# Performance work log

Hardware: AMD Instinct MI355X
Metric: run time of the kernel (lower is better)

Reference implementation:

```python
import jax, jax.numpy as jnp
import numpy as np

N_NODES = 50000
N_EDGES = 1600000
NEG_SLOPE = 0.2


def setup_inputs() -> dict:
    key = jax.random.key(0)
    ks = jax.random.split(key, 11)
    s = 0.1  # small init scale
    return {
        "x": jax.random.normal(ks[0], (N_NODES, 128), dtype=jnp.float32),
        "edge_index": jax.random.randint(ks[1], (2, N_EDGES), 0, N_NODES, dtype=jnp.int64),
        "W1": jax.random.normal(ks[2], (128, 128), dtype=jnp.float32) * s,
        "att_src1": jax.random.normal(ks[3], (2, 64), dtype=jnp.float32) * s,
        "att_dst1": jax.random.normal(ks[4], (2, 64), dtype=jnp.float32) * s,
        "b1": jax.random.normal(ks[5], (128,), dtype=jnp.float32) * s,
        "W2": jax.random.normal(ks[6], (128, 64), dtype=jnp.float32) * s,
        "att_src2": jax.random.normal(ks[7], (1, 64), dtype=jnp.float32) * s,
        "att_dst2": jax.random.normal(ks[8], (1, 64), dtype=jnp.float32) * s,
        "b2": jax.random.normal(ks[9], (64,), dtype=jnp.float32) * s,
    }


def gat_conv(x, W, a_src, a_dst, bias, src, dst, n_nodes):
    # x: [N, F_in]; W: [F_in, H*C]; a_src/a_dst: [H, C]; bias: [H*C]
    H, C = a_src.shape
    xl = (x @ W).reshape(n_nodes, H, C)                 # [N,H,C]
    alpha_s = jnp.einsum('nhc,hc->nh', xl, a_src)       # [N,H]
    alpha_d = jnp.einsum('nhc,hc->nh', xl, a_dst)       # [N,H]
    e = jax.nn.leaky_relu(alpha_s[src] + alpha_d[dst], NEG_SLOPE)  # [E,H]
    # segment softmax over edges sharing the same destination node
    m = jax.ops.segment_max(e, dst, num_segments=n_nodes)          # [N,H]
    m = jnp.where(jnp.isfinite(m), m, 0.0)
    e = jnp.exp(e - m[dst])
    denom = jax.ops.segment_sum(e, dst, num_segments=n_nodes)      # [N,H]
    alpha = e / denom[dst]                               # self-loops guarantee denom > 0
    msg = xl[src] * alpha[:, :, None]                    # [E,H,C]
    out = jax.ops.segment_sum(msg, dst, num_segments=n_nodes)      # [N,H,C]
    return out.reshape(n_nodes, H * C) + bias


def reference(x, edge_index, W1, att_src1, att_dst1, b1, W2, att_src2, att_dst2, b2):
    n = x.shape[0]
    # PyG GATConv default add_self_loops=True
    loops = jnp.arange(n, dtype=edge_index.dtype)
    src = jnp.concatenate([edge_index[0], loops])
    dst = jnp.concatenate([edge_index[1], loops])

    h = gat_conv(x, W1, att_src1, att_dst1, b1, src, dst, n)   # [N, 128]
    h = jax.nn.relu(h)                                          # dropout p=0 (eval)
    h = gat_conv(h, W2, att_src2, att_dst2, b2, src, dst, n)   # [N, 64]
    h = jax.nn.relu(h)
    return h
```

## Files before the change

### kernel.cpp

```cpp
#include <hip/hip_runtime.h>
#include <cstdint>
#include <cstddef>

#define NEG_SLOPE 0.2f

#define NB 128
#define LOG_NB 7
#define MAXK 512

__device__ inline unsigned short f2bf(float f) {
    unsigned int u = __float_as_uint(f);
    u += 0x7FFFu + ((u >> 16) & 1u);
    return (unsigned short)(u >> 16);
}
__device__ inline float bf2f(unsigned short u) {
    return __uint_as_float(((unsigned int)u) << 16);
}

__global__ __launch_bounds__(256) void sort_count_kernel(const int* __restrict__ ei, int E, int EE,
                                                         int K, int CH, int* __restrict__ bcnt) {
    __shared__ int hist[MAXK];
    int tid = threadIdx.x;
    for (int i = tid; i < K; i += 256) hist[i] = 0;
    __syncthreads();
    int lo = blockIdx.x * CH;
    int hi = lo + CH; if (hi > EE) hi = EE;
    for (int e = lo + tid; e < hi; e += 256) {
        int d = (e < E) ? ei[(size_t)E + e] : (e - E);
        atomicAdd(&hist[d >> LOG_NB], 1);
    }
    __syncthreads();
    for (int i = tid; i < K; i += 256)
        if (hist[i]) atomicAdd(&bcnt[i], hist[i]);
}

__global__ void sort_scan_kernel(const int* __restrict__ bcnt, int* __restrict__ boff,
                                 int* __restrict__ bcur, int K, int EE) {
    __shared__ int buf[MAXK];
    int tid = threadIdx.x;
    int v = (tid < K) ? bcnt[tid] : 0;
    buf[tid] = v;
    __syncthreads();
    for (int o = 1; o < MAXK; o <<= 1) {
        int t = (tid >= o) ? buf[tid - o] : 0;
        __syncthreads();
        buf[tid] += t;
        __syncthreads();
    }
    if (tid < K) {
        int ex = buf[tid] - v;
        boff[tid] = ex;
        bcur[tid] = ex;
    }
    if (tid == K) boff[K] = EE;
}

__global__ __launch_bounds__(256) void sort_scatter_kernel(const int* __restrict__ ei, int E, int EE,
                                                           int K, int CH, int* __restrict__ bcur,
                                                           unsigned int* __restrict__ bkt) {
    __shared__ int hist[MAXK];
    __shared__ int base[MAXK];
    int tid = threadIdx.x;
    for (int i = tid; i < K; i += 256) hist[i] = 0;
    __syncthreads();
    int lo = blockIdx.x * CH;
    int hi = lo + CH; if (hi > EE) hi = EE;
    for (int e = lo + tid; e < hi; e += 256) {
        int d = (e < E) ? ei[(size_t)E + e] : (e - E);
        atomicAdd(&hist[d >> LOG_NB], 1);
    }
    __syncthreads();
    for (int i = tid; i < K; i += 256) {
        int c = hist[i];
        base[i] = c ? atomicAdd(&bcur[i], c) : 0;
    }
    __syncthreads();
    for (int i = tid; i < K; i += 256) hist[i] = 0;
    __syncthreads();
    for (int e = lo + tid; e < hi; e += 256) {
        int s, d;
        if (e < E) { s = ei[e]; d = ei[(size_t)E + e]; }
        else       { s = e - E; d = e - E; }
        int k = d >> LOG_NB;
        int r = atomicAdd(&hist[k], 1);
        bkt[(size_t)base[k] + r] = (unsigned int)s | ((unsigned int)d << 16);
    }
}

__global__ __launch_bounds__(256) void sort_finalize_kernel(const unsigned int* __restrict__ bkt,
                                                            const int* __restrict__ boff,
                                                            int* __restrict__ off,
                                                            int* __restrict__ csrc, int N) {
    __shared__ int nhist[NB];
    __shared__ int loff[NB + 1];
    int k = blockIdx.x;
    int tid = threadIdx.x;
    int node0 = k << LOG_NB;
    int nh = N - node0; if (nh > NB) nh = NB;
    int beg = boff[k], end = boff[k + 1];
    for (int i = tid; i < NB; i += 256) nhist[i] = 0;
    __syncthreads();
    for (int e = beg + tid; e < end; e += 256)
        atomicAdd(&nhist[(bkt[e] >> 16) - node0], 1);
    __syncthreads();
    if (tid == 0) {
        int run = beg;
        for (int i = 0; i < nh; i++) { loff[i] = run; run += nhist[i]; }
        loff[nh] = run;
    }
    __syncthreads();
    for (int i = tid; i < nh; i += 256) off[node0 + i] = loff[i];
    if (node0 + nh == N && tid == 0) off[N] = loff[nh];
    for (int i = tid; i < nh; i += 256) nhist[i] = loff[i];
    __syncthreads();
    for (int e = beg + tid; e < end; e += 256) {
        unsigned int p = bkt[e];
        int pos = atomicAdd(&nhist[(p >> 16) - node0], 1);
        csrc[pos] = (int)(p & 0xFFFFu);
    }
}


template <int FOUT, int H>
__global__ __launch_bounds__(256) void gemm_att_kernel(const float* __restrict__ X,
                                                       const float* __restrict__ W,
                                                       const float* __restrict__ attS,
                                                       const float* __restrict__ attD,
                                                       unsigned short* __restrict__ Ybf,
                                                       float* __restrict__ as_,
                                                       float* __restrict__ ad_, int N) {
    __shared__ float sW[64 * FOUT];
    __shared__ float sX[16 * 128];
    int tid = threadIdx.x;
    size_t rowbase = (size_t)blockIdx.x * 16;
    const float* xp = X + rowbase * 128;
    for (int i = tid; i < 16 * 128; i += 256) sX[i] = xp[i];

    constexpr int RPT = (16 * FOUT) / 256;
    int col = tid % FOUT;
    int rg  = tid / FOUT;
    int r0  = rg * RPT;
    float acc[RPT];
#pragma unroll
    for (int i = 0; i < RPT; i++) acc[i] = 0.f;

    for (int k0 = 0; k0 < 128; k0 += 64) {
        __syncthreads();
        for (int i = tid; i < 64 * FOUT; i += 256) sW[i] = W[(size_t)k0 * FOUT + i];
        __syncthreads();
#pragma unroll 4
        for (int k = 0; k < 64; k++) {
            float wv = sW[k * FOUT + col];
#pragma unroll
            for (int i = 0; i < RPT; i++)
                acc[i] += sX[(r0 + i) * 128 + k0 + k] * wv;
        }
    }
    unsigned short* yp = Ybf + rowbase * FOUT;
#pragma unroll
    for (int i = 0; i < RPT; i++) yp[(size_t)(r0 + i) * FOUT + col] = f2bf(acc[i]);

    int lane = tid & 63;
    int head = col >> 6;
    float asv = attS[col];
    float adv = attD[col];
#pragma unroll
    for (int i = 0; i < RPT; i++) {
        float ps = acc[i] * asv;
        float pd = acc[i] * adv;
#pragma unroll
        for (int o = 32; o; o >>= 1) { ps += __shfl_xor(ps, o); pd += __shfl_xor(pd, o); }
        if (lane == 0) {
            size_t row = rowbase + r0 + i;
            as_[row * H + head] = ps;
            ad_[row * H + head] = pd;
        }
    }
}


template <int H>
__global__ __launch_bounds__(256) void agg_kernel(const unsigned short* __restrict__ xl,
                                                  const float* __restrict__ as_,
                                                  const float* __restrict__ ad_,
                                                  const float* __restrict__ bias,
                                                  const int* __restrict__ off,
                                                  const int* __restrict__ csrc,
                                                  float* __restrict__ out, int NH) {
    __shared__ float2 sps[4][64];
    int wiw  = threadIdx.x >> 6;
    int lane = threadIdx.x & 63;
    int wid  = blockIdx.x * 4 + wiw;
    if (wid >= NH) return;
    int node = wid / H;
    int head = wid - node * H;
    int beg = off[node], end = off[node + 1];
    int deg = end - beg;
    float adn = ad_[wid];

    int c   = lane & 15;
    int sub = lane >> 4;
    float4 acc = make_float4(0.f, 0.f, 0.f, 0.f);
    const ushort4* xq = (const ushort4*)xl + head * 16 + c;

    if (deg <= 64) {
        int s = 0;
        float t = -1e30f;
        if (lane < deg) {
            s = csrc[beg + lane];
            t = as_[s * H + head] + adn;
            t = t > 0.f ? t : NEG_SLOPE * t;
        }
        float m = t;
#pragma unroll
        for (int o = 32; o; o >>= 1) m = fmaxf(m, __shfl_xor(m, o));
        float ev = (lane < deg) ? __expf(t - m) : 0.f;
        float sum = ev;
#pragma unroll
        for (int o = 32; o; o >>= 1) sum += __shfl_xor(sum, o);
        float p = ev * (1.f / sum);
        sps[wiw][lane] = make_float2(p, __int_as_float(s));
        int iters = (deg + 3) >> 2;
#pragma unroll 8
        for (int j = 0; j < iters; j++) {
            float2 q = sps[wiw][j * 4 + sub];
            float a  = q.x;
            int   sj = __float_as_int(q.y);
            ushort4 v = xq[(size_t)sj * (H * 16)];
            acc.x = fmaf(a, bf2f(v.x), acc.x);
            acc.y = fmaf(a, bf2f(v.y), acc.y);
            acc.z = fmaf(a, bf2f(v.z), acc.z);
            acc.w = fmaf(a, bf2f(v.w), acc.w);
        }
    } else {
        float m = -1e30f;
        for (int b = beg; b < end; b += 64) {
            int e = b + lane;
            float v = -1e30f;
            if (e < end) {
                int s = csrc[e];
                float t = as_[s * H + head] + adn;
                v = t > 0.f ? t : NEG_SLOPE * t;
            }
            m = fmaxf(m, v);
        }
#pragma unroll
        for (int o = 32; o; o >>= 1) m = fmaxf(m, __shfl_xor(m, o));

        float sum = 0.f;
        for (int b = beg; b < end; b += 64) {
            int e = b + lane;
            if (e < end) {
                int s = csrc[e];
                float t = as_[s * H + head] + adn;
                t = t > 0.f ? t : NEG_SLOPE * t;
                sum += __expf(t - m);
            }
        }
#pragma unroll
        for (int o = 32; o; o >>= 1) sum += __shfl_xor(sum, o);
        float inv = 1.f / sum;

        for (int b = beg; b < end; b += 64) {
            int cnt = end - b; if (cnt > 64) cnt = 64;
            float p = 0.f; int s = 0;
            if (lane < cnt) {
                s = csrc[b + lane];
                float t = as_[s * H + head] + adn;
                t = t > 0.f ? t : NEG_SLOPE * t;
                p = __expf(t - m) * inv;
            }
            sps[wiw][lane] = make_float2(p, __int_as_float(s));
            int iters = (cnt + 3) >> 2;
#pragma unroll 8
            for (int j = 0; j < iters; j++) {
                float2 q = sps[wiw][j * 4 + sub];
                float a  = q.x;
                int   sj = __float_as_int(q.y);
                ushort4 v = xq[(size_t)sj * (H * 16)];
                acc.x = fmaf(a, bf2f(v.x), acc.x);
                acc.y = fmaf(a, bf2f(v.y), acc.y);
                acc.z = fmaf(a, bf2f(v.z), acc.z);
                acc.w = fmaf(a, bf2f(v.w), acc.w);
            }
        }
    }

#pragma unroll
    for (int o = 16; o <= 32; o <<= 1) {
        acc.x += __shfl_xor(acc.x, o);
        acc.y += __shfl_xor(acc.y, o);
        acc.z += __shfl_xor(acc.z, o);
        acc.w += __shfl_xor(acc.w, o);
    }
    if (sub == 0) {
        const float4 bq = ((const float4*)(bias + head * 64))[c];
        float4 o4;
        o4.x = fmaxf(acc.x + bq.x, 0.f);
        o4.y = fmaxf(acc.y + bq.y, 0.f);
        o4.z = fmaxf(acc.z + bq.z, 0.f);
        o4.w = fmaxf(acc.w + bq.w, 0.f);
        ((float4*)(out + (size_t)node * (H * 64) + head * 64))[c] = o4;
    }
}


extern "C" void kernel_launch(void* const* d_in, const int* in_sizes, int n_in,
                              void* d_out, int out_size, void* d_ws, size_t ws_size,
                              hipStream_t stream) {
    const float* x        = (const float*)d_in[0];
    const int*   ei       = (const int*)d_in[1];
    const float* W1       = (const float*)d_in[2];
    const float* attS1    = (const float*)d_in[3];
    const float* attD1    = (const float*)d_in[4];
    const float* b1       = (const float*)d_in[5];
    const float* W2       = (const float*)d_in[6];
    const float* attS2    = (const float*)d_in[7];
    const float* attD2    = (const float*)d_in[8];
    const float* b2       = (const float*)d_in[9];
    float* out            = (float*)d_out;

    int N  = in_sizes[0] / 128;
    int E  = in_sizes[1] / 2;
    int EE = E + N;
    int K  = (N + NB - 1) >> LOG_NB;

    char* w = (char*)d_ws;
    auto alloc = [&](size_t bytes) -> void* {
        void* p = (void*)w;
        w += (bytes + 255) & ~(size_t)255;
        return p;
    };
    int*   bcnt = (int*)alloc((size_t)(K + 1) * 4);
    int*   boff = (int*)alloc((size_t)(K + 1) * 4);
    int*   bcur = (int*)alloc((size_t)(K + 1) * 4);
    int*   off  = (int*)alloc((size_t)(N + 1) * 4);
    int*   csrc = (int*)alloc((size_t)EE * 4);
    unsigned short* xl1 = (unsigned short*)alloc((size_t)N * 128 * 2);
    float* sd1  = (float*)alloc((size_t)N * 2 * 4);
    float* dd1  = (float*)alloc((size_t)N * 2 * 4);
    float* h1   = (float*)alloc((size_t)N * 128 * 4);

    unsigned int* bkt = (unsigned int*)xl1;
    unsigned short* xl2 = xl1;
    float* sd2 = sd1;
    float* dd2 = dd1;

    hipMemsetAsync(bcnt, 0, (size_t)(K + 1) * 4, stream);

    int G  = 256;
    int CH = (EE + G - 1) / G;
    sort_count_kernel<<<G, 256, 0, stream>>>(ei, E, EE, K, CH, bcnt);
    sort_scan_kernel<<<1, MAXK, 0, stream>>>(bcnt, boff, bcur, K, EE);
    sort_scatter_kernel<<<G, 256, 0, stream>>>(ei, E, EE, K, CH, bcur, bkt);
    sort_finalize_kernel<<<K, 256, 0, stream>>>(bkt, boff, off, csrc, N);

    gemm_att_kernel<128, 2><<<(N + 15) / 16, 256, 0, stream>>>(x, W1, attS1, attD1, xl1, sd1, dd1, N);
    agg_kernel<2><<<(N * 2 + 3) / 4, 256, 0, stream>>>(xl1, sd1, dd1, b1, off, csrc, h1, N * 2);

    gemm_att_kernel<64, 1><<<(N + 15) / 16, 256, 0, stream>>>(h1, W2, attS2, attD2, xl2, sd2, dd2, N);
    agg_kernel<1><<<(N + 3) / 4, 256, 0, stream>>>(xl2, sd2, dd2, b2, off, csrc, out, N);
}
```

Measured before the change: 345.5 us.

## Register-tile GEMM, merge heads per wave in aggregation, widen sort buckets

The GEMM now computes an 8x4 register tile per thread over a larger row block, using float4 LDS reads and bounds checks. The layer-1 aggregation handles both heads in one wave per node, computing both softmaxes together and gathering 16-byte bf16 rows. The layer-2 aggregation uses 8 lanes per edge with uint4 loads. The sort bucket width grows from 128 to 512 nodes, which may change the sort-finalize shared-memory behaviour. These changes aim to cut redundant index and score loads and raise memory-access width, at the cost of higher register pressure.

```diff
diff --git a/kernel.cpp b/kernel.cpp
--- a/kernel.cpp
+++ b/kernel.cpp
@@ -4,8 +4,8 @@
 
 #define NEG_SLOPE 0.2f
 
-#define NB 128
-#define LOG_NB 7
+#define NB 512
+#define LOG_NB 9
 #define MAXK 512
 
 __device__ inline unsigned short f2bf(float f) {
@@ -13,9 +13,8 @@
     u += 0x7FFFu + ((u >> 16) & 1u);
     return (unsigned short)(u >> 16);
 }
-__device__ inline float bf2f(unsigned short u) {
-    return __uint_as_float(((unsigned int)u) << 16);
-}
+__device__ inline float bf_lo(unsigned int u) { return __uint_as_float(u << 16); }
+__device__ inline float bf_hi(unsigned int u) { return __uint_as_float(u & 0xFFFF0000u); }
 
 __global__ __launch_bounds__(256) void sort_count_kernel(const int* __restrict__ ei, int E, int EE,
                                                          int K, int CH, int* __restrict__ bcnt) {
@@ -129,86 +128,236 @@
                                                        unsigned short* __restrict__ Ybf,
                                                        float* __restrict__ as_,
                                                        float* __restrict__ ad_, int N) {
+    constexpr int ROWS = 8192 / FOUT;
+    constexpr int CG   = FOUT / 4;
+    __shared__ float sX[ROWS][68];
     __shared__ float sW[64 * FOUT];
-    __shared__ float sX[16 * 128];
     int tid = threadIdx.x;
-    size_t rowbase = (size_t)blockIdx.x * 16;
-    const float* xp = X + rowbase * 128;
-    for (int i = tid; i < 16 * 128; i += 256) sX[i] = xp[i];
-
-    constexpr int RPT = (16 * FOUT) / 256;
-    int col = tid % FOUT;
-    int rg  = tid / FOUT;
-    int r0  = rg * RPT;
-    float acc[RPT];
-#pragma unroll
-    for (int i = 0; i < RPT; i++) acc[i] = 0.f;
+    int rowbase = blockIdx.x * ROWS;
+    int cg = tid % CG;
+    int rg = tid / CG;
+    int r0 = rg * 8;
+
+    float acc[8][4];
+#pragma unroll
+    for (int i = 0; i < 8; i++)
+#pragma unroll
+        for (int c = 0; c < 4; c++) acc[i][c] = 0.f;
 
     for (int k0 = 0; k0 < 128; k0 += 64) {
         __syncthreads();
-        for (int i = tid; i < 64 * FOUT; i += 256) sW[i] = W[(size_t)k0 * FOUT + i];
+        for (int idx = tid; idx < ROWS * 64; idx += 256) {
+            int r = idx >> 6, kk = idx & 63;
+            int row = rowbase + r;
+            sX[r][kk] = (row < N) ? X[(size_t)row * 128 + k0 + kk] : 0.f;
+        }
+        for (int idx = tid; idx < 64 * FOUT; idx += 256)
+            sW[idx] = W[(size_t)k0 * FOUT + idx];
         __syncthreads();
-#pragma unroll 4
-        for (int k = 0; k < 64; k++) {
-            float wv = sW[k * FOUT + col];
-#pragma unroll
-            for (int i = 0; i < RPT; i++)
-                acc[i] += sX[(r0 + i) * 128 + k0 + k] * wv;
-        }
-    }
-    unsigned short* yp = Ybf + rowbase * FOUT;
-#pragma unroll
-    for (int i = 0; i < RPT; i++) yp[(size_t)(r0 + i) * FOUT + col] = f2bf(acc[i]);
-
-    int lane = tid & 63;
-    int head = col >> 6;
-    float asv = attS[col];
-    float adv = attD[col];
-#pragma unroll
-    for (int i = 0; i < RPT; i++) {
-        float ps = acc[i] * asv;
-        float pd = acc[i] * adv;
-#pragma unroll
-        for (int o = 32; o; o >>= 1) { ps += __shfl_xor(ps, o); pd += __shfl_xor(pd, o); }
-        if (lane == 0) {
-            size_t row = rowbase + r0 + i;
-            as_[row * H + head] = ps;
-            ad_[row * H + head] = pd;
-        }
-    }
-}
-
-
-template <int H>
-__global__ __launch_bounds__(256) void agg_kernel(const unsigned short* __restrict__ xl,
-                                                  const float* __restrict__ as_,
-                                                  const float* __restrict__ ad_,
-                                                  const float* __restrict__ bias,
-                                                  const int* __restrict__ off,
-                                                  const int* __restrict__ csrc,
-                                                  float* __restrict__ out, int NH) {
+        for (int k = 0; k < 64; k += 4) {
+            float4 xr[8];
+#pragma unroll
+            for (int i = 0; i < 8; i++)
+                xr[i] = *(const float4*)&sX[r0 + i][k];
+#pragma unroll
+            for (int kk = 0; kk < 4; kk++) {
+                float4 wv = ((const float4*)(sW + (size_t)(k + kk) * FOUT))[cg];
+#pragma unroll
+                for (int i = 0; i < 8; i++) {
+                    float xv = (&xr[i].x)[kk];
+                    acc[i][0] = fmaf(xv, wv.x, acc[i][0]);
+                    acc[i][1] = fmaf(xv, wv.y, acc[i][1]);
+                    acc[i][2] = fmaf(xv, wv.z, acc[i][2]);
+                    acc[i][3] = fmaf(xv, wv.w, acc[i][3]);
+                }
+            }
+        }
+    }
+
+#pragma unroll
+    for (int i = 0; i < 8; i++) {
+        int row = rowbase + r0 + i;
+        if (row < N) {
+            ushort4 v;
+            v.x = f2bf(acc[i][0]); v.y = f2bf(acc[i][1]);
+            v.z = f2bf(acc[i][2]); v.w = f2bf(acc[i][3]);
+            *(ushort4*)(Ybf + (size_t)row * FOUT + cg * 4) = v;
+        }
+    }
+
+    float4 asv = ((const float4*)attS)[cg];
+    float4 adv = ((const float4*)attD)[cg];
+    int head = (H == 2) ? (cg >> 4) : 0;
+#pragma unroll
+    for (int i = 0; i < 8; i++) {
+        float ps = acc[i][0] * asv.x + acc[i][1] * asv.y + acc[i][2] * asv.z + acc[i][3] * asv.w;
+        float pd = acc[i][0] * adv.x + acc[i][1] * adv.y + acc[i][2] * adv.z + acc[i][3] * adv.w;
+#pragma unroll
+        for (int o = 1; o <= 8; o <<= 1) { ps += __shfl_xor(ps, o); pd += __shfl_xor(pd, o); }
+        int row = rowbase + r0 + i;
+        if ((tid & 15) == 0 && row < N) {
+            as_[(size_t)row * H + head] = ps;
+            ad_[(size_t)row * H + head] = pd;
+        }
+    }
+}
+
+
+__global__ __launch_bounds__(256) void agg1_kernel(const unsigned short* __restrict__ xl,
+                                                   const float* __restrict__ as_,
+                                                   const float* __restrict__ ad_,
+                                                   const float* __restrict__ bias,
+                                                   const int* __restrict__ off,
+                                                   const int* __restrict__ csrc,
+                                                   float* __restrict__ out, int N) {
+    __shared__ float4 sps[4][64];
+    int wiw  = threadIdx.x >> 6;
+    int lane = threadIdx.x & 63;
+    int node = blockIdx.x * 4 + wiw;
+    if (node >= N) return;
+    int beg = off[node], end = off[node + 1];
+    int deg = end - beg;
+    float2 adn = ((const float2*)ad_)[node];
+
+    int cl  = lane & 15;
+    int sub = lane >> 4;
+    int hd1 = (cl >> 3) & 1;
+    float acc[8];
+#pragma unroll
+    for (int i = 0; i < 8; i++) acc[i] = 0.f;
+    const uint4* xq = (const uint4*)xl + cl;
+
+    if (deg <= 64) {
+        int s = 0;
+        float t0 = -1e30f, t1 = -1e30f;
+        if (lane < deg) {
+            s = csrc[beg + lane];
+            float2 asv = ((const float2*)as_)[s];
+            t0 = asv.x + adn.x; t0 = t0 > 0.f ? t0 : NEG_SLOPE * t0;
+            t1 = asv.y + adn.y; t1 = t1 > 0.f ? t1 : NEG_SLOPE * t1;
+        }
+        float m0 = t0, m1 = t1;
+#pragma unroll
+        for (int o = 32; o; o >>= 1) {
+            m0 = fmaxf(m0, __shfl_xor(m0, o));
+            m1 = fmaxf(m1, __shfl_xor(m1, o));
+        }
+        float e0 = (lane < deg) ? __expf(t0 - m0) : 0.f;
+        float e1 = (lane < deg) ? __expf(t1 - m1) : 0.f;
+        float s0 = e0, s1 = e1;
+#pragma unroll
+        for (int o = 32; o; o >>= 1) { s0 += __shfl_xor(s0, o); s1 += __shfl_xor(s1, o); }
+        sps[wiw][lane] = make_float4(e0 / s0, e1 / s1, __int_as_float(s), 0.f);
+        int iters = (deg + 3) >> 2;
+#pragma unroll 8
+        for (int j = 0; j < iters; j++) {
+            float4 q = sps[wiw][j * 4 + sub];
+            float a  = hd1 ? q.y : q.x;
+            int   sj = __float_as_int(q.z);
+            uint4 v  = xq[(size_t)sj * 16];
+            acc[0] = fmaf(a, bf_lo(v.x), acc[0]); acc[1] = fmaf(a, bf_hi(v.x), acc[1]);
+            acc[2] = fmaf(a, bf_lo(v.y), acc[2]); acc[3] = fmaf(a, bf_hi(v.y), acc[3]);
+            acc[4] = fmaf(a, bf_lo(v.z), acc[4]); acc[5] = fmaf(a, bf_hi(v.z), acc[5]);
+            acc[6] = fmaf(a, bf_lo(v.w), acc[6]); acc[7] = fmaf(a, bf_hi(v.w), acc[7]);
+        }
+    } else {
+        float m0 = -1e30f, m1 = -1e30f;
+        for (int b = beg; b < end; b += 64) {
+            int e = b + lane;
+            if (e < end) {
+                int s = csrc[e];
+                float2 asv = ((const float2*)as_)[s];
+                float t0 = asv.x + adn.x; t0 = t0 > 0.f ? t0 : NEG_SLOPE * t0;
+                float t1 = asv.y + adn.y; t1 = t1 > 0.f ? t1 : NEG_SLOPE * t1;
+                m0 = fmaxf(m0, t0); m1 = fmaxf(m1, t1);
+            }
+        }
+#pragma unroll
+        for (int o = 32; o; o >>= 1) {
+            m0 = fmaxf(m0, __shfl_xor(m0, o));
+            m1 = fmaxf(m1, __shfl_xor(m1, o));
+        }
+        float s0 = 0.f, s1 = 0.f;
+        for (int b = beg; b < end; b += 64) {
+            int e = b + lane;
+            if (e < end) {
+                int s = csrc[e];
+                float2 asv = ((const float2*)as_)[s];
+                float t0 = asv.x + adn.x; t0 = t0 > 0.f ? t0 : NEG_SLOPE * t0;
+                float t1 = asv.y + adn.y; t1 = t1 > 0.f ? t1 : NEG_SLOPE * t1;
+                s0 += __expf(t0 - m0); s1 += __expf(t1 - m1);
+            }
+        }
+#pragma unroll
+        for (int o = 32; o; o >>= 1) { s0 += __shfl_xor(s0, o); s1 += __shfl_xor(s1, o); }
+        float i0 = 1.f / s0, i1 = 1.f / s1;
+        for (int b = beg; b < end; b += 64) {
+            int cnt = end - b; if (cnt > 64) cnt = 64;
+            float p0 = 0.f, p1 = 0.f; int s = 0;
+            if (lane < cnt) {
+                s = csrc[b + lane];
+                float2 asv = ((const float2*)as_)[s];
+                float t0 = asv.x + adn.x; t0 = t0 > 0.f ? t0 : NEG_SLOPE * t0;
+                float t1 = asv.y + adn.y; t1 = t1 > 0.f ? t1 : NEG_SLOPE * t1;
+                p0 = __expf(t0 - m0) * i0; p1 = __expf(t1 - m1) * i1;
+            }
+            sps[wiw][lane] = make_float4(p0, p1, __int_as_float(s), 0.f);
+            int iters = (cnt + 3) >> 2;
+#pragma unroll 8
+            for (int j = 0; j < iters; j++) {
+                float4 q = sps[wiw][j * 4 + sub];
+                float a  = hd1 ? q.y : q.x;
+                int   sj = __float_as_int(q.z);
+                uint4 v  = xq[(size_t)sj * 16];
+                acc[0] = fmaf(a, bf_lo(v.x), acc[0]); acc[1] = fmaf(a, bf_hi(v.x), acc[1]);
+                acc[2] = fmaf(a, bf_lo(v.y), acc[2]); acc[3] = fmaf(a, bf_hi(v.y), acc[3]);
+                acc[4] = fmaf(a, bf_lo(v.z), acc[4]); acc[5] = fmaf(a, bf_hi(v.z), acc[5]);
+                acc[6] = fmaf(a, bf_lo(v.w), acc[6]); acc[7] = fmaf(a, bf_hi(v.w), acc[7]);
+            }
+        }
+    }
+#pragma unroll
+    for (int o = 16; o <= 32; o <<= 1)
+#pragma unroll
+        for (int i = 0; i < 8; i++) acc[i] += __shfl_xor(acc[i], o);
+    if (sub == 0) {
+        float* op = out + (size_t)node * 128 + cl * 8;
+        const float* bp = bias + cl * 8;
+#pragma unroll
+        for (int i = 0; i < 8; i++) op[i] = fmaxf(acc[i] + bp[i], 0.f);
+    }
+}
+
+
+__global__ __launch_bounds__(256) void agg2_kernel(const unsigned short* __restrict__ xl,
+                                                   const float* __restrict__ as_,
+                                                   const float* __restrict__ ad_,
+                                                   const float* __restrict__ bias,
+                                                   const int* __restrict__ off,
+                                                   const int* __restrict__ csrc,
+                                                   float* __restrict__ out, int N) {
     __shared__ float2 sps[4][64];
     int wiw  = threadIdx.x >> 6;
     int lane = threadIdx.x & 63;
-    int wid  = blockIdx.x * 4 + wiw;
-    if (wid >= NH) return;
-    int node = wid / H;
-    int head = wid - node * H;
+    int node = blockIdx.x * 4 + wiw;
+    if (node >= N) return;
     int beg = off[node], end = off[node + 1];
     int deg = end - beg;
-    float adn = ad_[wid];
-
-    int c   = lane & 15;
-    int sub = lane >> 4;
-    float4 acc = make_float4(0.f, 0.f, 0.f, 0.f);
-    const ushort4* xq = (const ushort4*)xl + head * 16 + c;
+    float adn = ad_[node];
+
+    int cl  = lane & 7;
+    int sub = lane >> 3;
+    float acc[8];
+#pragma unroll
+    for (int i = 0; i < 8; i++) acc[i] = 0.f;
+    const uint4* xq = (const uint4*)xl + cl;
 
     if (deg <= 64) {
         int s = 0;
         float t = -1e30f;
         if (lane < deg) {
             s = csrc[beg + lane];
-            t = as_[s * H + head] + adn;
+            t = as_[s] + adn;
             t = t > 0.f ? t : NEG_SLOPE * t;
         }
         float m = t;
@@ -218,41 +367,36 @@
         float sum = ev;
 #pragma unroll
         for (int o = 32; o; o >>= 1) sum += __shfl_xor(sum, o);
-        float p = ev * (1.f / sum);
-        sps[wiw][lane] = make_float2(p, __int_as_float(s));
-        int iters = (deg + 3) >> 2;
+        sps[wiw][lane] = make_float2(ev / sum, __int_as_float(s));
+        int iters = (deg + 7) >> 3;
 #pragma unroll 8
         for (int j = 0; j < iters; j++) {
-            float2 q = sps[wiw][j * 4 + sub];
+            float2 q = sps[wiw][j * 8 + sub];
             float a  = q.x;
             int   sj = __float_as_int(q.y);
-            ushort4 v = xq[(size_t)sj * (H * 16)];
-            acc.x = fmaf(a, bf2f(v.x), acc.x);
-            acc.y = fmaf(a, bf2f(v.y), acc.y);
-            acc.z = fmaf(a, bf2f(v.z), acc.z);
-            acc.w = fmaf(a, bf2f(v.w), acc.w);
+            uint4 v  = xq[(size_t)sj * 8];
+            acc[0] = fmaf(a, bf_lo(v.x), acc[0]); acc[1] = fmaf(a, bf_hi(v.x), acc[1]);
+            acc[2] = fmaf(a, bf_lo(v.y), acc[2]); acc[3] = fmaf(a, bf_hi(v.y), acc[3]);
+            acc[4] = fmaf(a, bf_lo(v.z), acc[4]); acc[5] = fmaf(a, bf_hi(v.z), acc[5]);
+            acc[6] = fmaf(a, bf_lo(v.w), acc[6]); acc[7] = fmaf(a, bf_hi(v.w), acc[7]);
         }
     } else {
         float m = -1e30f;
         for (int b = beg; b < end; b += 64) {
             int e = b + lane;
-            float v = -1e30f;
             if (e < end) {
-                int s = csrc[e];
-                float t = as_[s * H + head] + adn;
-                v = t > 0.f ? t : NEG_SLOPE * t;
-            }
-            m = fmaxf(m, v);
+                float t = as_[csrc[e]] + adn;
+                t = t > 0.f ? t : NEG_SLOPE * t;
+                m = fmaxf(m, t);
+            }
         }
 #pragma unroll
         for (int o = 32; o; o >>= 1) m = fmaxf(m, __shfl_xor(m, o));
-
         float sum = 0.f;
         for (int b = beg; b < end; b += 64) {
             int e = b + lane;
             if (e < end) {
-                int s = csrc[e];
-                float t = as_[s * H + head] + adn;
+                float t = as_[csrc[e]] + adn;
                 t = t > 0.f ? t : NEG_SLOPE * t;
                 sum += __expf(t - m);
             }
@@ -260,47 +404,39 @@
 #pragma unroll
         for (int o = 32; o; o >>= 1) sum += __shfl_xor(sum, o);
         float inv = 1.f / sum;
-
         for (int b = beg; b < end; b += 64) {
             int cnt = end - b; if (cnt > 64) cnt = 64;
             float p = 0.f; int s = 0;
             if (lane < cnt) {
                 s = csrc[b + lane];
-                float t = as_[s * H + head] + adn;
+                float t = as_[s] + adn;
                 t = t > 0.f ? t : NEG_SLOPE * t;
                 p = __expf(t - m) * inv;
             }
             sps[wiw][lane] = make_float2(p, __int_as_float(s));
-            int iters = (cnt + 3) >> 2;
+            int iters = (cnt + 7) >> 3;
 #pragma unroll 8
             for (int j = 0; j < iters; j++) {
-                float2 q = sps[wiw][j * 4 + sub];
+                float2 q = sps[wiw][j * 8 + sub];
                 float a  = q.x;
                 int   sj = __float_as_int(q.y);
-                ushort4 v = xq[(size_t)sj * (H * 16)];
-                acc.x = fmaf(a, bf2f(v.x), acc.x);
-                acc.y = fmaf(a, bf2f(v.y), acc.y);
-                acc.z = fmaf(a, bf2f(v.z), acc.z);
-                acc.w = fmaf(a, bf2f(v.w), acc.w);
-            }
-        }
-    }
-
-#pragma unroll
-    for (int o = 16; o <= 32; o <<= 1) {
-        acc.x += __shfl_xor(acc.x, o);
-        acc.y += __shfl_xor(acc.y, o);
-        acc.z += __shfl_xor(acc.z, o);
-        acc.w += __shfl_xor(acc.w, o);
-    }
+                uint4 v  = xq[(size_t)sj * 8];
+                acc[0] = fmaf(a, bf_lo(v.x), acc[0]); acc[1] = fmaf(a, bf_hi(v.x), acc[1]);
+                acc[2] = fmaf(a, bf_lo(v.y), acc[2]); acc[3] = fmaf(a, bf_hi(v.y), acc[3]);
+                acc[4] = fmaf(a, bf_lo(v.z), acc[4]); acc[5] = fmaf(a, bf_hi(v.z), acc[5]);
+                acc[6] = fmaf(a, bf_lo(v.w), acc[6]); acc[7] = fmaf(a, bf_hi(v.w), acc[7]);
+            }
+        }
+    }
+#pragma unroll
+    for (int o = 8; o <= 32; o <<= 1)
+#pragma unroll
+        for (int i = 0; i < 8; i++) acc[i] += __shfl_xor(acc[i], o);
     if (sub == 0) {
-        const float4 bq = ((const float4*)(bias + head * 64))[c];
-        float4 o4;
-        o4.x = fmaxf(acc.x + bq.x, 0.f);
-        o4.y = fmaxf(acc.y + bq.y, 0.f);
-        o4.z = fmaxf(acc.z + bq.z, 0.f);
-        o4.w = fmaxf(acc.w + bq.w, 0.f);
-        ((float4*)(out + (size_t)node * (H * 64) + head * 64))[c] = o4;
+        float* op = out + (size_t)node * 64 + cl * 8;
+        const float* bp = bias + cl * 8;
+#pragma unroll
+        for (int i = 0; i < 8; i++) op[i] = fmaxf(acc[i] + bp[i], 0.f);
     }
 }
 
@@ -355,9 +491,9 @@
     sort_scatter_kernel<<<G, 256, 0, stream>>>(ei, E, EE, K, CH, bcur, bkt);
     sort_finalize_kernel<<<K, 256, 0, stream>>>(bkt, boff, off, csrc, N);
 
-    gemm_att_kernel<128, 2><<<(N + 15) / 16, 256, 0, stream>>>(x, W1, attS1, attD1, xl1, sd1, dd1, N);
-    agg_kernel<2><<<(N * 2 + 3) / 4, 256, 0, stream>>>(xl1, sd1, dd1, b1, off, csrc, h1, N * 2);
-
-    gemm_att_kernel<64, 1><<<(N + 15) / 16, 256, 0, stream>>>(h1, W2, attS2, attD2, xl2, sd2, dd2, N);
-    agg_kernel<1><<<(N + 3) / 4, 256, 0, stream>>>(xl2, sd2, dd2, b2, off, csrc, out, N);
-}
+    gemm_att_kernel<128, 2><<<(N + 63) / 64, 256, 0, stream>>>(x, W1, attS1, attD1, xl1, sd1, dd1, N);
+    agg1_kernel<<<(N + 3) / 4, 256, 0, stream>>>(xl1, sd1, dd1, b1, off, csrc, h1, N);
+
+    gemm_att_kernel<64, 1><<<(N + 127) / 128, 256, 0, stream>>>(h1, W2, attS2, attD2, xl2, sd2, dd2, N);
+    agg2_kernel<<<(N + 3) / 4, 256, 0, stream>>>(xl2, sd2, dd2, b2, off, csrc, out, N);
+}
```

New measurement: 377.3 us. +9.2%, slower.
